# Optimization experiments

Measured on AMD Instinct MI355X. Metric: run time of the kernel, lower is better.

Reference implementation:

```python
import jax, jax.numpy as jnp
import numpy as np

BITS_I, BITS_W = 8, 8
GROUP = 36
DIR_I = (0, 1, 2, 3)
DIR_W = (0, 1, 2, 3)


def bfp_quantize(x, bits, group_size, perm):
    """Block floating point: groups of `group_size` elements (after permuting
    axes by `perm` and flattening) share one exponent (exponent of max abs);
    mantissas are rounded to `bits` signed bits."""
    inv_perm = tuple(np.argsort(perm))
    xp = jnp.transpose(x, perm)
    shape = xp.shape
    flat = xp.reshape(-1)
    n = flat.shape[0]
    pad = (-n) % group_size
    flat = jnp.pad(flat, (0, pad))
    g = flat.reshape(-1, group_size)
    maxabs = jnp.max(jnp.abs(g), axis=1, keepdims=True)
    e = jnp.floor(jnp.log2(jnp.maximum(maxabs, jnp.float32(1e-38))))
    scale = jnp.exp2(e - (bits - 1))  # shared group exponent, `bits` mantissa bits
    qmax = 2 ** (bits - 1) - 1
    q = jnp.clip(jnp.round(g / scale), -qmax - 1, qmax) * scale
    q = jnp.where(maxabs == 0, jnp.float32(0), q)
    out = q.reshape(-1)[:n].reshape(shape)
    return jnp.transpose(out, inv_perm)


def conv2d(x, w, b, stride=1, padding=1, dilation=1, groups=1):
    out = jax.lax.conv_general_dilated(
        x, w,
        window_strides=(stride, stride),
        padding=[(padding, padding), (padding, padding)],
        rhs_dilation=(dilation, dilation),
        feature_group_count=groups,
        dimension_numbers=('NCHW', 'OIHW', 'NCHW'))
    if b is not None:
        out = out + b[None, :, None, None]
    return out


def setup_inputs() -> dict:
    key = jax.random.key(0)
    k1, k2, k3 = jax.random.split(key, 3)
    x = jax.random.normal(k1, (16, 256, 56, 56), dtype=jnp.float32)
    fan_in = 256 * 3 * 3
    bound = 1.0 / np.sqrt(fan_in)
    weight = jax.random.uniform(k2, (256, 256, 3, 3), dtype=jnp.float32,
                                minval=-np.sqrt(6.0 / fan_in), maxval=np.sqrt(6.0 / fan_in))
    bias = jax.random.uniform(k3, (256,), dtype=jnp.float32, minval=-bound, maxval=bound)
    return {"x": x, "weight": weight, "bias": bias}


def reference(x, weight, bias):
    xq = bfp_quantize(x, BITS_I, GROUP, DIR_I)
    wq = bfp_quantize(weight, BITS_W, GROUP, DIR_W)
    return conv2d(xq, wq, bias, stride=1, padding=1, dilation=1, groups=1)
```

## Files before the change

### kernel.cpp

```cpp
#include <hip/hip_runtime.h>

typedef short short8 __attribute__((ext_vector_type(8)));
typedef float f32x4 __attribute__((ext_vector_type(4)));
typedef unsigned short u16;
typedef __attribute__((address_space(3))) unsigned lds_u32_t;
typedef __attribute__((address_space(1))) const unsigned glb_u32_t;

namespace {
constexpr int NIMG = 16;
constexpr int CIN  = 256;
constexpr int HIMG = 56;
constexpr int WIMG = 56;
constexpr int KOUT = 256;
constexpr int PIX  = HIMG * WIMG;
constexpr int HPAD = 58;
constexpr int PP   = HPAD * HPAD;
constexpr int TILES = 26;
constexpr int NX   = NIMG * CIN * PIX;
constexpr int NWEL = KOUT * CIN * 9;
constexpr int XQ_HALVES = NIMG * 32 * PP * 8;
constexpr int MAXB = XQ_HALVES - 8;
constexpr int CHUNK = 8 * PIX;
constexpr int XBLK = NIMG * 32;
constexpr int WB   = 64;
}

__global__ __launch_bounds__(256) void quant_fused(
        const float* __restrict__ x, u16* __restrict__ xq2,
        const float* __restrict__ wsrc, u16* __restrict__ wt3) {
    __shared__ u16 ot[CHUNK];
    const int b = blockIdx.x;
    const int t = threadIdx.x;

    if (b < XBLK) {
        const long s  = (long)b * CHUNK;
        const int  g0 = (int)(s / 36);
        const int  g1 = (int)((s + CHUNK - 1) / 36);

        if (t < 228) {
            int ph, pw;
            if (t < 58)       { ph = 0;  pw = t; }
            else if (t < 116) { ph = 57; pw = t - 58; }
            else { int r = t - 116; ph = 1 + (r >> 1); pw = (r & 1) * 57; }
            *(uint4*)(xq2 + ((size_t)b * PP + ph * HPAD + pw) * 8) =
                make_uint4(0, 0, 0, 0);
        }

        for (int g = g0 + t; g <= g1; g += 256) {
            const long e0 = (long)g * 36;
            float v[36];
            if (e0 + 36 <= (long)NX) {
                const float4* p4 = (const float4*)(x + e0);
#pragma unroll
                for (int j = 0; j < 9; j++) {
                    float4 q4 = p4[j];
                    v[4*j+0] = q4.x; v[4*j+1] = q4.y;
                    v[4*j+2] = q4.z; v[4*j+3] = q4.w;
                }
            } else {
                for (int j = 0; j < 36; j++)
                    v[j] = (e0 + j < (long)NX) ? x[e0 + j] : 0.f;
            }
            float ma = 0.f;
#pragma unroll
            for (int j = 0; j < 36; j++) ma = fmaxf(ma, fabsf(v[j]));
            float scale = 0.f, rinv = 0.f;
            if (ma != 0.f) {
                float e = floorf(log2f(ma));
                scale = exp2f(e - 7.f);
                rinv  = exp2f(7.f - e);
            }
            const long o = e0 - s;
#pragma unroll
            for (int j = 0; j < 36; j += 2) {
                float qa = fminf(fmaxf(rintf(v[j]   * rinv), -128.f), 127.f) * scale;
                float qb = fminf(fmaxf(rintf(v[j+1] * rinv), -128.f), 127.f) * scale;
                uint pk = (__float_as_uint(qa) >> 16)
                        | ((__float_as_uint(qb) >> 16) << 16);
                long oo = o + j;
                if (oo >= 0 && oo < CHUNK)
                    *(uint*)&ot[oo] = pk;
            }
        }
        __syncthreads();

        for (int p = t; p < PIX; p += 256) {
            short8 o8;
#pragma unroll
            for (int cl = 0; cl < 8; cl++)
                o8[cl] = (short)ot[cl * PIX + p];
            int ph = p / WIMG + 1, pw = p % WIMG + 1;
            *(short8*)(xq2 + ((size_t)b * PP + ph * HPAD + pw) * 8) = o8;
        }
    } else {
        int g = (b - XBLK) * 256 + t;
        int base = g * 36;
        float v[36];
        const float4* p4 = (const float4*)(wsrc + base);
#pragma unroll
        for (int j = 0; j < 9; j++) {
            float4 tt = p4[j];
            v[4*j+0] = tt.x; v[4*j+1] = tt.y; v[4*j+2] = tt.z; v[4*j+3] = tt.w;
        }
        float ma = 0.f;
#pragma unroll
        for (int j = 0; j < 36; j++) ma = fmaxf(ma, fabsf(v[j]));
        float scale = 0.f, rinv = 0.f;
        if (ma != 0.f) {
            float e = floorf(log2f(ma));
            scale = exp2f(e - 7.f);
            rinv  = exp2f(7.f - e);
        }
        int k  = g >> 6;
        int c0 = (g & 63) * 4;
#pragma unroll
        for (int j = 0; j < 36; j++) {
            float q = rintf(v[j] * rinv);
            q = fminf(fmaxf(q, -128.f), 127.f) * scale;
            int c  = c0 + j / 9;
            int rs = j % 9;
            int idx = ((((rs * 4 + (c >> 6)) * 8 + ((c >> 3) & 7)) * KOUT) + k) * 8 + (c & 7);
            wt3[idx] = (u16)(__float_as_uint(q) >> 16);
        }
    }
}

#define ISSUE3(csp_, rs_, sub_, qb_)                                           \
    {                                                                          \
        const int xoff8_ = (((rs_) / 3) * HPAD + ((rs_) % 3)) * 8;             \
        const int sA_ = ((rs_) * 4 + (csp_)) * 16384 + (sub_) * 8192;          \
        const int sB_ = ((csp_) * 8 + (sub_) * 4) * PP * 8;                    \
        _Pragma("unroll")                                                      \
        for (int hl = 0; hl < 2; hl++) {                                       \
            __builtin_amdgcn_global_load_lds(                                  \
                (glb_u32_t*)(wt3 + sA_ + hl * 512 + aLw),                      \
                (lds_u32_t*)(lA3[qb_] + hl * 512 + dstw),                      \
                16, 0, 0);                                                     \
            int bi_ = bBw + sB_ + xoff8_ + hl * 512;                           \
            bi_ = min(bi_, MAXB);       \
            __builtin_amdgcn_global_load_lds(                                  \
                (glb_u32_t*)(xq2 + bi_),                                       \
                (lds_u32_t*)(lB3[qb_] + hl * 512 + dstw),                      \
                16, 0, 0);                                                     \
        }                                                                      \
    }

__global__ __launch_bounds__(256) void conv_kernel(
        const u16* __restrict__ xq2, const u16* __restrict__ wt3,
        const float* __restrict__ bias, float* __restrict__ out) {
    __shared__ u16 lA3[3][4096];
    __shared__ u16 lB3[3][4096];

    const int tid  = threadIdx.x;
    const int lane = tid & 63;
    const int wv   = tid >> 6;
    const int bx   = blockIdx.x;
    const int n    = bx / TILES;
    const int t0   = (bx % TILES) * 128;
    const int k0   = blockIdx.y * 128;

    const int aLw  = (k0 + lane) * 8 + wv * 2048;
    const int bBw  = ((n * 32 + wv) * PP + t0 + lane) * 8;
    const int dstw = wv * 1024 + lane * 8;

    const int frow = lane & 15;
    const int fkk  = lane >> 4;
    const int fAo = (fkk * 128 + (wv >> 1) * 64 + frow) * 8;
    const int fBo = (fkk * 128 + (wv & 1) * 64 + frow) * 8;

    f32x4 acc[4][4] = {};

    ISSUE3(0, 0, 0, 0);
    ISSUE3(0, 0, 1, 1);

#pragma unroll
    for (int h = 0; h < 72; h++) {
        if (h < 71) asm volatile("s_waitcnt vmcnt(4)" ::: "memory");
        else        asm volatile("s_waitcnt vmcnt(0)" ::: "memory");
        __builtin_amdgcn_s_barrier();
        __builtin_amdgcn_sched_barrier(0);

        const int hb = h % 3;
        short8 af[4], bf[4];
#pragma unroll
        for (int i = 0; i < 4; i++)
            af[i] = *(const short8*)(lA3[hb] + fAo + i * 128);
#pragma unroll
        for (int j = 0; j < 4; j++)
            bf[j] = *(const short8*)(lB3[hb] + fBo + j * 128);

        __builtin_amdgcn_s_setprio(1);
#pragma unroll
        for (int i = 0; i < 4; i++)
#pragma unroll
            for (int j = 0; j < 4; j++)
                acc[i][j] = __builtin_amdgcn_mfma_f32_16x16x32_bf16(
                    af[i], bf[j], acc[i][j], 0, 0, 0);
        __builtin_amdgcn_s_setprio(0);
        __builtin_amdgcn_sched_barrier(0);

        if (h + 2 < 72) {
            const int h2 = h + 2;
            ISSUE3(h2 / 18, (h2 / 2) % 9, h2 & 1, h2 % 3);
        }
    }

    const int kbase = k0 + (wv >> 1) * 64 + fkk * 4;
    const int mbase = (wv & 1) * 64 + frow;
#pragma unroll
    for (int j = 0; j < 4; j++) {
        int ppp = t0 + mbase + j * 16;
        int h = ppp / HPAD, w = ppp % HPAD;
        if (w < WIMG && h < HIMG) {
            float* ob = out + (size_t)n * KOUT * PIX + h * WIMG + w;
#pragma unroll
            for (int i = 0; i < 4; i++) {
                int kch = kbase + i * 16;
#pragma unroll
                for (int r = 0; r < 4; r++)
                    ob[(size_t)(kch + r) * PIX] = acc[i][j][r] + bias[kch + r];
            }
        }
    }
}

extern "C" void kernel_launch(void* const* d_in, const int* in_sizes, int n_in,
                              void* d_out, int out_size, void* d_ws, size_t ws_size,
                              hipStream_t stream) {
    const float* x   = (const float*)d_in[0];
    const float* wgt = (const float*)d_in[1];
    const float* bs  = (const float*)d_in[2];
    float* out = (float*)d_out;

    u16* xq2 = (u16*)d_ws;
    u16* wt3 = xq2 + XQ_HALVES;

    quant_fused<<<XBLK + WB, 256, 0, stream>>>(x, xq2, wgt, wt3);
    conv_kernel<<<dim3(NIMG * TILES, 2), 256, 0, stream>>>(xq2, wt3, bs, out);
}
```

Baseline: 186.8 us.

## Stage input halo once per channel slab in LDS and stream weights to registers

Replaces the per-step triple-buffered LDS staging of both weight and input tiles with a single LDS load of an input slab, covering 64 channels and 256 padded pixels, per channel-slab stage. All nine filter taps are read from that slab by offset, so each input element is fetched from global memory once per slab instead of once per tap. Weights are loaded directly into registers with a three-deep rotating register prefetch. The cost is that the input load is no longer overlapped with compute: each slab stage waits on vmcnt(0) plus barriers, and register pressure rises from holding three weight fragments.

```diff
diff --git a/kernel.cpp b/kernel.cpp
--- a/kernel.cpp
+++ b/kernel.cpp
@@ -19,7 +19,6 @@
 constexpr int NX   = NIMG * CIN * PIX;
 constexpr int NWEL = KOUT * CIN * 9;
 constexpr int XQ_HALVES = NIMG * 32 * PP * 8;
-constexpr int MAXB = XQ_HALVES - 8;
 constexpr int CHUNK = 8 * PIX;
 constexpr int XBLK = NIMG * 32;
 constexpr int WB   = 64;
@@ -125,31 +124,21 @@
     }
 }
 
-#define ISSUE3(csp_, rs_, sub_, qb_)                                           \
+#define LOADA(dst_, c_)                                                        \
     {                                                                          \
-        const int xoff8_ = (((rs_) / 3) * HPAD + ((rs_) % 3)) * 8;             \
-        const int sA_ = ((rs_) * 4 + (csp_)) * 16384 + (sub_) * 8192;          \
-        const int sB_ = ((csp_) * 8 + (sub_) * 4) * PP * 8;                    \
+        const int csp_ = (c_) / 18;                                            \
+        const int rsk_ = ((c_) % 18) / 2;                                      \
+        const int sub_ = (c_) & 1;                                             \
+        const u16* ap_ = wt3 + (rsk_ * 4 + csp_) * 16384 + sub_ * 8192;        \
         _Pragma("unroll")                                                      \
-        for (int hl = 0; hl < 2; hl++) {                                       \
-            __builtin_amdgcn_global_load_lds(                                  \
-                (glb_u32_t*)(wt3 + sA_ + hl * 512 + aLw),                      \
-                (lds_u32_t*)(lA3[qb_] + hl * 512 + dstw),                      \
-                16, 0, 0);                                                     \
-            int bi_ = bBw + sB_ + xoff8_ + hl * 512;                           \
-            bi_ = min(bi_, MAXB);       \
-            __builtin_amdgcn_global_load_lds(                                  \
-                (glb_u32_t*)(xq2 + bi_),                                       \
-                (lds_u32_t*)(lB3[qb_] + hl * 512 + dstw),                      \
-                16, 0, 0);                                                     \
-        }                                                                      \
+        for (int i_ = 0; i_ < 4; i_++)                                         \
+            dst_[i_] = *(const short8*)(ap_ + aOff + i_ * 128);                \
     }
 
 __global__ __launch_bounds__(256) void conv_kernel(
         const u16* __restrict__ xq2, const u16* __restrict__ wt3,
         const float* __restrict__ bias, float* __restrict__ out) {
-    __shared__ u16 lA3[3][4096];
-    __shared__ u16 lB3[3][4096];
+    __shared__ u16 lB[16384];
 
     const int tid  = threadIdx.x;
     const int lane = tid & 63;
@@ -159,49 +148,64 @@
     const int t0   = (bx % TILES) * 128;
     const int k0   = blockIdx.y * 128;
 
-    const int aLw  = (k0 + lane) * 8 + wv * 2048;
-    const int bBw  = ((n * 32 + wv) * PP + t0 + lane) * 8;
-    const int dstw = wv * 1024 + lane * 8;
-
     const int frow = lane & 15;
     const int fkk  = lane >> 4;
-    const int fAo = (fkk * 128 + (wv >> 1) * 64 + frow) * 8;
-    const int fBo = (fkk * 128 + (wv & 1) * 64 + frow) * 8;
+    const int aOff = fkk * 2048 + (k0 + (wv >> 1) * 64 + frow) * 8;
+    const int bcol = (wv & 1) * 64 + frow;
 
     f32x4 acc[4][4] = {};
-
-    ISSUE3(0, 0, 0, 0);
-    ISSUE3(0, 0, 1, 1);
-
-#pragma unroll
-    for (int h = 0; h < 72; h++) {
-        if (h < 71) asm volatile("s_waitcnt vmcnt(4)" ::: "memory");
-        else        asm volatile("s_waitcnt vmcnt(0)" ::: "memory");
+    short8 a0[4], a1[4], a2[4];
+
+    LOADA(a0, 0);
+    LOADA(a1, 1);
+    LOADA(a2, 2);
+
+#pragma unroll
+    for (int s = 0; s < 4; s++) {
         __builtin_amdgcn_s_barrier();
-        __builtin_amdgcn_sched_barrier(0);
-
-        const int hb = h % 3;
-        short8 af[4], bf[4];
-#pragma unroll
-        for (int i = 0; i < 4; i++)
-            af[i] = *(const short8*)(lA3[hb] + fAo + i * 128);
-#pragma unroll
-        for (int j = 0; j < 4; j++)
-            bf[j] = *(const short8*)(lB3[hb] + fBo + j * 128);
-
-        __builtin_amdgcn_s_setprio(1);
-#pragma unroll
-        for (int i = 0; i < 4; i++)
+#pragma unroll
+        for (int l = 0; l < 8; l++) {
+            const int oct = wv * 2 + (l >> 2);
+            const int q   = l & 3;
+            __builtin_amdgcn_global_load_lds(
+                (glb_u32_t*)(xq2 + ((size_t)(n * 32 + s * 8 + oct) * PP
+                                    + t0 + q * 64 + lane) * 8),
+                (lds_u32_t*)(lB + oct * 2048 + q * 512 + lane * 8),
+                16, 0, 0);
+        }
+        asm volatile("s_waitcnt vmcnt(0)" ::: "memory");
+        __builtin_amdgcn_s_barrier();
+
+#pragma unroll
+        for (int k = 0; k < 18; k++) {
+            const int c   = 18 * s + k;
+            const int rs  = k >> 1;
+            const int sub = k & 1;
+            const int doff = (rs / 3) * HPAD + (rs % 3);
+
+            if (k >= 3) asm volatile("s_waitcnt vmcnt(8)" ::: "memory");
+
+            short8 bf[4];
 #pragma unroll
             for (int j = 0; j < 4; j++)
-                acc[i][j] = __builtin_amdgcn_mfma_f32_16x16x32_bf16(
-                    af[i], bf[j], acc[i][j], 0, 0, 0);
-        __builtin_amdgcn_s_setprio(0);
-        __builtin_amdgcn_sched_barrier(0);
-
-        if (h + 2 < 72) {
-            const int h2 = h + 2;
-            ISSUE3(h2 / 18, (h2 / 2) % 9, h2 & 1, h2 % 3);
+                bf[j] = *(const short8*)(lB + (sub * 4 + fkk) * 2048
+                                         + (doff + bcol + j * 16) * 8);
+
+            __builtin_amdgcn_s_setprio(1);
+#pragma unroll
+            for (int i = 0; i < 4; i++)
+#pragma unroll
+                for (int j = 0; j < 4; j++)
+                    acc[i][j] = __builtin_amdgcn_mfma_f32_16x16x32_bf16(
+                        (k % 3 == 0) ? a0[i] : (k % 3 == 1) ? a1[i] : a2[i],
+                        bf[j], acc[i][j], 0, 0, 0);
+            __builtin_amdgcn_s_setprio(0);
+
+            if (c + 3 < 72) {
+                if (k % 3 == 0)      LOADA(a0, c + 3)
+                else if (k % 3 == 1) LOADA(a1, c + 3)
+                else                 LOADA(a2, c + 3)
+            }
         }
     }
 
```

Measured after the change: 163.8 us. 12.4% less time.
